# Kernel optimization log

Measured on AMD Instinct MI355X. Metric: run time of the kernel, lower is better.

## Reference

```python
import jax, jax.numpy as jnp
import numpy as np

N = 200000    # nodes
DMAX = 32     # max in-degree (padded)
F = 128       # in_feats
H = 128       # lstm hidden == in_feats (use_pp=False)
OUT = 128     # out_feats


def setup_inputs() -> dict:
    key = jax.random.key(0)
    ks = jax.random.split(key, 11)
    u = lambda k, shape, s: jax.random.uniform(k, shape, jnp.float32, -s, s)
    feat = jax.random.normal(ks[0], (N, F), jnp.float32)
    # norms come from sqrt(degree) in the original; keep them positive, O(1)
    in_norm = jax.random.uniform(ks[1], (N,), jnp.float32) + 1.0
    out_norm = jax.random.uniform(ks[2], (N,), jnp.float32) + 1.0
    neighbors = jax.random.randint(ks[3], (N, DMAX), 0, N, jnp.int32)
    degrees = jax.random.randint(ks[4], (N,), 1, DMAX + 1, jnp.int32)
    s_lstm = 1.0 / np.sqrt(H)   # torch LSTM default init scale
    s_lin = 1.0 / np.sqrt(F)    # module's reset_parameters scale
    W_ih = u(ks[5], (4 * H, F), s_lstm)
    W_hh = u(ks[6], (4 * H, H), s_lstm)
    b_ih = u(ks[7], (4 * H,), s_lstm)
    b_hh = u(ks[8], (4 * H,), s_lstm)
    W_lin = u(ks[9], (OUT, F), s_lin)
    b_lin = u(ks[10], (OUT,), s_lin)
    return dict(feat=feat, in_norm=in_norm, out_norm=out_norm,
                W_ih=W_ih, W_hh=W_hh, b_ih=b_ih, b_hh=b_hh,
                W_lin=W_lin, b_lin=b_lin,
                neighbors=neighbors, degrees=degrees)


def reference(feat, in_norm, out_norm, W_ih, W_hh, b_ih, b_hh, W_lin, b_lin,
              neighbors, degrees):
    # graph.nodes['_U'].data['h'] = feat / out_norm
    msg_src = feat / out_norm[:, None]                      # [N, F]
    n, dmax = neighbors.shape
    h_dim = W_hh.shape[1]
    step_mask = jnp.arange(dmax)[None, :] < degrees[:, None]  # [N, DMAX]

    def step(carry, xs):
        h, c = carry
        idx_t, m_t = xs                                      # [N], [N]
        x = msg_src[idx_t]                                   # gather messages [N, F]
        gates = x @ W_ih.T + b_ih + h @ W_hh.T + b_hh        # [N, 4H]
        i, f, g, o = jnp.split(gates, 4, axis=-1)
        i = jax.nn.sigmoid(i)
        f = jax.nn.sigmoid(f)
        o = jax.nn.sigmoid(o)
        g = jnp.tanh(g)
        c_new = f * c + i * g
        h_new = o * jnp.tanh(c_new)
        m = m_t[:, None]
        return (jnp.where(m, h_new, h), jnp.where(m, c_new, c)), None

    init = (jnp.zeros((n, h_dim), feat.dtype), jnp.zeros((n, h_dim), feat.dtype))
    (h_final, _), _ = jax.lax.scan(step, init, (neighbors.T, step_mask.T))
    # feat = linear(h / in_norm)
    return (h_final / in_norm[:, None]) @ W_lin.T + b_lin
```

## Files before the change

kernel.cpp:

```cpp
#include <hip/hip_runtime.h>

#define NN 200000
#define NB 64
#define NWG (NN / NB)

typedef unsigned short u16;
typedef unsigned int u32;
typedef __attribute__((ext_vector_type(8))) short short8;
typedef __attribute__((ext_vector_type(4))) float f32x4;

#define LOG2E 1.4426950408889634f
#define TWOLOG2E 2.8853900817779268f

__device__ __forceinline__ u16 f2bf(float x) {
  u32 u = __float_as_uint(x);
  u += 0x7FFFu + ((u >> 16) & 1u);
  return (u16)(u >> 16);
}

__global__ void k_prep_msg(const float* __restrict__ feat, const float* __restrict__ onorm,
                           u16* __restrict__ msg) {
  int i = blockIdx.x * 256 + threadIdx.x;
  int row = i >> 4, c8 = (i & 15) * 8;
  const float4 a = *(const float4*)(feat + (size_t)row * 128 + c8);
  const float4 b = *(const float4*)(feat + (size_t)row * 128 + c8 + 4);
  float s = 1.0f / onorm[row];
  short8 v = { (short)f2bf(a.x * s), (short)f2bf(a.y * s), (short)f2bf(a.z * s), (short)f2bf(a.w * s),
               (short)f2bf(b.x * s), (short)f2bf(b.y * s), (short)f2bf(b.z * s), (short)f2bf(b.w * s) };
  *(short8*)(msg + (size_t)row * 128 + c8) = v;
}

__global__ void k_prep_w(const float* __restrict__ Wih, const float* __restrict__ Whh,
                         const float* __restrict__ Wlin, const float* __restrict__ bih,
                         const float* __restrict__ bhh, u16* __restrict__ wihb,
                         u16* __restrict__ whhb, u16* __restrict__ wlinb,
                         float* __restrict__ bsum) {
  int i = blockIdx.x * 256 + threadIdx.x;
  if (i < 65536) {
    int gate = i >> 14;
    float s = (gate == 2) ? TWOLOG2E : -LOG2E;
    wihb[i] = f2bf(Wih[i] * s);
  } else if (i < 131072) {
    int j = i - 65536;
    int gate = j >> 14;
    float s = (gate == 2) ? TWOLOG2E : -LOG2E;
    whhb[j] = f2bf(Whh[j] * s);
  } else if (i < 147456) {
    wlinb[i - 131072] = f2bf(Wlin[i - 131072]);
  } else {
    int j = i - 147456;
    float s = ((j >> 7) == 2) ? TWOLOG2E : -LOG2E;
    bsum[j] = (bih[j] + bhh[j]) * s;
  }
}

__global__ void k_hist(const int* __restrict__ degs, int* __restrict__ hist, int n) {
  __shared__ int lh[33];
  if (threadIdx.x < 33) lh[threadIdx.x] = 0;
  __syncthreads();
  int i = blockIdx.x * 256 + threadIdx.x;
  if (i < n) atomicAdd(&lh[degs[i]], 1);
  __syncthreads();
  if (threadIdx.x < 33 && lh[threadIdx.x]) atomicAdd(&hist[threadIdx.x], lh[threadIdx.x]);
}

__global__ void k_scan(const int* __restrict__ hist, int* __restrict__ basep) {
  if (threadIdx.x == 0 && blockIdx.x == 0) {
    int a = 0;
    for (int d = 32; d >= 1; --d) { basep[d] = a; a += hist[d]; }
    basep[0] = a;
  }
}

__global__ void k_scatter(const int* __restrict__ degs, int* __restrict__ basep,
                          int* __restrict__ perm, int n) {
  __shared__ int lh[33], lbase[33], lc[33];
  int t = threadIdx.x;
  if (t < 33) { lh[t] = 0; lc[t] = 0; }
  __syncthreads();
  int i = blockIdx.x * 256 + t;
  int d = (i < n) ? degs[i] : 0;
  if (i < n) atomicAdd(&lh[d], 1);
  __syncthreads();
  if (t < 33 && lh[t]) lbase[t] = atomicAdd(&basep[t], lh[t]);
  __syncthreads();
  if (i < n) { int r = atomicAdd(&lc[d], 1); perm[lbase[d] + r] = i; }
}

__global__ __launch_bounds__(512, 2) void k_main(
    const u16* __restrict__ msg, const u16* __restrict__ wihb,
    const u16* __restrict__ whhb, const u16* __restrict__ wlinb,
    const float* __restrict__ bsum, const float* __restrict__ blin,
    const float* __restrict__ inorm, const int* __restrict__ nbrs,
    const int* __restrict__ degs, const int* __restrict__ perm,
    float* __restrict__ out) {
  __shared__ alignas(16) u16 Xl[2][64 * 136];
  __shared__ alignas(16) u16 Hl[2][64 * 136];
  __shared__ int gidl[64];

  const int tid = threadIdx.x;
  const int w = tid >> 6;
  const int lane = tid & 63;
  const int l15 = lane & 15;
  const int g4 = lane >> 4;
  const int w16 = w * 16;
  const int gr = tid >> 4;
  const int gc = (tid & 15) * 8;
  const int base = blockIdx.x * NB;

  if (tid < NB) gidl[tid] = perm[base + tid];
  {
    u32* hz = (u32*)Hl[0];
#pragma unroll
    for (int s = 0; s < 8; ++s) hz[tid + s * 512] = 0;
    if (tid < 256) hz[tid + 4096] = 0;
  }
  __syncthreads();

  const int gid0 = gidl[gr], gid1 = gidl[gr + 32];
  const int* nb0 = nbrs + (size_t)gid0 * 32;
  const int* nb1 = nbrs + (size_t)gid1 * 32;

  short8 fih[4][4], fhh[4][4];
#pragma unroll
  for (int g = 0; g < 4; ++g)
#pragma unroll
    for (int kk = 0; kk < 4; ++kk) {
      size_t o = (size_t)(g * 128 + w16 + l15) * 128 + kk * 32 + g4 * 8;
      fih[g][kk] = *(const short8*)(wihb + o);
      fhh[g][kk] = *(const short8*)(whhb + o);
    }
  float bias[4];
#pragma unroll
  for (int g = 0; g < 4; ++g) bias[g] = bsum[g * 128 + w16 + l15];

  u32 dgp[4];
#pragma unroll
  for (int r = 0; r < 4; ++r) {
    u32 p = 0;
#pragma unroll
    for (int q = 0; q < 4; ++q) p |= ((u32)degs[gidl[r * 16 + g4 * 4 + q]]) << (8 * q);
    dgp[r] = p;
  }
  const int maxdeg = degs[gidl[0]];

  {
    int i0 = nb0[0], i1 = nb1[0];
    short8 p0 = *(const short8*)(msg + (size_t)i0 * 128 + gc);
    short8 p1 = *(const short8*)(msg + (size_t)i1 * 128 + gc);
    *(short8*)(&Xl[0][gr * 136 + gc]) = p0;
    *(short8*)(&Xl[0][(gr + 32) * 136 + gc]) = p1;
  }
  int ni0 = 0, ni1 = 0;
  if (maxdeg > 1) { ni0 = nb0[1]; ni1 = nb1[1]; }

  float c[4][4] = {};
  u16 hbf[4][4] = {};
  __syncthreads();

  int cur = 0;
  for (int t = 0; t < maxdeg; ++t) {
    const int nxt = cur ^ 1;
    short8 pf0, pf1;
    if (t + 1 < maxdeg) {
      pf0 = *(const short8*)(msg + (size_t)ni0 * 128 + gc);
      pf1 = *(const short8*)(msg + (size_t)ni1 * 128 + gc);
    }
    if (t + 2 < maxdeg) { ni0 = nb0[t + 2]; ni1 = nb1[t + 2]; }

    const u16* Xc = &Xl[cur][0];
    const u16* Hc = &Hl[cur][0];

#pragma unroll
    for (int rp = 0; rp < 2; ++rp) {
      f32x4 acc[2][4];
#pragma unroll
      for (int r = 0; r < 2; ++r)
#pragma unroll
        for (int g = 0; g < 4; ++g) acc[r][g] = (f32x4){bias[g], bias[g], bias[g], bias[g]};

#pragma unroll
      for (int rf = 0; rf < 2; ++rf) {
        short8 ax[4];
#pragma unroll
        for (int kk = 0; kk < 4; ++kk)
          ax[kk] = *(const short8*)(&Xc[(rp * 32 + rf * 16 + l15) * 136 + kk * 32 + g4 * 8]);
#pragma unroll
        for (int kk = 0; kk < 4; ++kk)
#pragma unroll
          for (int g = 0; g < 4; ++g)
            acc[rf][g] = __builtin_amdgcn_mfma_f32_16x16x32_bf16(ax[kk], fih[g][kk], acc[rf][g], 0, 0, 0);
      }
#pragma unroll
      for (int rf = 0; rf < 2; ++rf) {
        short8 ah[4];
#pragma unroll
        for (int kk = 0; kk < 4; ++kk)
          ah[kk] = *(const short8*)(&Hc[(rp * 32 + rf * 16 + l15) * 136 + kk * 32 + g4 * 8]);
#pragma unroll
        for (int kk = 0; kk < 4; ++kk)
#pragma unroll
          for (int g = 0; g < 4; ++g)
            acc[rf][g] = __builtin_amdgcn_mfma_f32_16x16x32_bf16(ah[kk], fhh[g][kk], acc[rf][g], 0, 0, 0);
      }

#pragma unroll
      for (int r = 0; r < 2; ++r) {
        const int rr = rp * 2 + r;
#pragma unroll
        for (int q = 0; q < 4; ++q) {
          float ei = __builtin_amdgcn_exp2f(acc[r][0][q]);
          float ef = __builtin_amdgcn_exp2f(acc[r][1][q]);
          float eg = __builtin_amdgcn_exp2f(acc[r][2][q]);
          float eo = __builtin_amdgcn_exp2f(acc[r][3][q]);
          float fv  = __builtin_amdgcn_rcpf(1.0f + ef);
          float rig = __builtin_amdgcn_rcpf((1.0f + ei) * (1.0f + eg));
          float ig  = (eg - 1.0f) * rig;
          float cn  = fv * c[rr][q] + ig;
          float ec  = __builtin_amdgcn_exp2f(cn * TWOLOG2E);
          float rho = __builtin_amdgcn_rcpf((1.0f + eo) * (1.0f + ec));
          float hn  = (ec - 1.0f) * rho;
          bool act = (int)((dgp[rr] >> (8 * q)) & 255u) > t;
          c[rr][q] = act ? cn : c[rr][q];
          hbf[rr][q] = act ? f2bf(hn) : hbf[rr][q];
        }
      }
    }

    if (t + 1 < maxdeg) {
      *(short8*)(&Xl[nxt][gr * 136 + gc]) = pf0;
      *(short8*)(&Xl[nxt][(gr + 32) * 136 + gc]) = pf1;
    }
#pragma unroll
    for (int rr = 0; rr < 4; ++rr)
#pragma unroll
      for (int q = 0; q < 4; ++q)
        Hl[nxt][(rr * 16 + g4 * 4 + q) * 136 + w16 + l15] = hbf[rr][q];
    __syncthreads();
    cur = nxt;
  }

  const u16* Hf = &Hl[cur][0];

  short8 wl[4];
#pragma unroll
  for (int kk = 0; kk < 4; ++kk)
    wl[kk] = *(const short8*)(wlinb + (size_t)(w16 + l15) * 128 + kk * 32 + g4 * 8);
  f32x4 a2[4] = {};
#pragma unroll
  for (int kk = 0; kk < 4; ++kk)
#pragma unroll
    for (int r = 0; r < 4; ++r) {
      short8 ah = *(const short8*)(&Hf[(r * 16 + l15) * 136 + kk * 32 + g4 * 8]);
      a2[r] = __builtin_amdgcn_mfma_f32_16x16x32_bf16(ah, wl[kk], a2[r], 0, 0, 0);
    }
  float blv = blin[w16 + l15];
#pragma unroll
  for (int r = 0; r < 4; ++r)
#pragma unroll
    for (int q = 0; q < 4; ++q) {
      int nl = r * 16 + g4 * 4 + q;
      int g = gidl[nl];
      out[(size_t)g * 128 + w16 + l15] = a2[r][q] / inorm[g] + blv;
    }
}

extern "C" void kernel_launch(void* const* d_in, const int* in_sizes, int n_in,
                              void* d_out, int out_size, void* d_ws, size_t ws_size,
                              hipStream_t stream) {
  const float* feat    = (const float*)d_in[0];
  const float* in_norm = (const float*)d_in[1];
  const float* out_nrm = (const float*)d_in[2];
  const float* W_ih    = (const float*)d_in[3];
  const float* W_hh    = (const float*)d_in[4];
  const float* b_ih    = (const float*)d_in[5];
  const float* b_hh    = (const float*)d_in[6];
  const float* W_lin   = (const float*)d_in[7];
  const float* b_lin   = (const float*)d_in[8];
  const int* neighbors = (const int*)d_in[9];
  const int* degrees   = (const int*)d_in[10];
  float* out = (float*)d_out;

  char* ws = (char*)d_ws;
  u16* msg    = (u16*)(ws);
  u16* wihb   = (u16*)(ws + 51200000);
  u16* whhb   = (u16*)(ws + 51331072);
  u16* wlinb  = (u16*)(ws + 51462144);
  float* bsum = (float*)(ws + 51494912);
  int* perm   = (int*)(ws + 51496960);
  int* hist   = (int*)(ws + 52296960);
  int* basep  = hist + 64;
  if (ws_size < 52297600) return;

  hipMemsetAsync(hist, 0, 64 * 4, stream);
  k_prep_msg<<<12500, 256, 0, stream>>>(feat, out_nrm, msg);
  k_prep_w<<<578, 256, 0, stream>>>(W_ih, W_hh, W_lin, b_ih, b_hh, wihb, whhb, wlinb, bsum);
  k_hist<<<782, 256, 0, stream>>>(degrees, hist, NN);
  k_scan<<<1, 1, 0, stream>>>(hist, basep);
  k_scatter<<<782, 256, 0, stream>>>(degrees, basep, perm, NN);
  k_main<<<NWG, 512, 0, stream>>>(msg, wihb, whhb, wlinb, bsum, b_lin, in_norm,
                                  neighbors, degrees, perm, out);
}
```

Measured before the change: 1.070 ms.

## Double LSTM node tile per workgroup and interleave gathers with MFMA row blocks

Each workgroup now processes 128 nodes instead of 64, so every block amortises its register-resident W_ih/W_hh fragments over twice as many rows. The inner loop walks 8 row blocks one at a time, raises wave priority around the MFMA sections, and spreads the next-step message gathers and LDS stores across specific row blocks. New h values are written to LDS as soon as each block finishes rather than in a batch at the end. LDS use doubles to roughly 140 KB and register pressure rises, which may cut occupancy below the two blocks per CU requested. Padding the last block and sharing one maxdeg across 128 degree-sorted nodes may also add wasted steps.

New measurement: 2.497 ms. 133% more time.

```diff
diff --git a/kernel.cpp b/kernel.cpp
--- a/kernel.cpp
+++ b/kernel.cpp
@@ -1,8 +1,8 @@
 #include <hip/hip_runtime.h>
 
 #define NN 200000
-#define NB 64
-#define NWG (NN / NB)
+#define NB 128
+#define NWG ((NN + NB - 1) / NB)
 
 typedef unsigned short u16;
 typedef unsigned int u32;
@@ -94,9 +94,9 @@
     const float* __restrict__ inorm, const int* __restrict__ nbrs,
     const int* __restrict__ degs, const int* __restrict__ perm,
     float* __restrict__ out) {
-  __shared__ alignas(16) u16 Xl[2][64 * 136];
-  __shared__ alignas(16) u16 Hl[2][64 * 136];
-  __shared__ int gidl[64];
+  __shared__ alignas(16) u16 Xl[2][128 * 136];
+  __shared__ alignas(16) u16 Hl[2][128 * 136];
+  __shared__ int gidl[128];
 
   const int tid = threadIdx.x;
   const int w = tid >> 6;
@@ -108,18 +108,23 @@
   const int gc = (tid & 15) * 8;
   const int base = blockIdx.x * NB;
 
-  if (tid < NB) gidl[tid] = perm[base + tid];
+  if (tid < NB) {
+    int idx = base + tid;
+    gidl[tid] = perm[idx < NN ? idx : NN - 1];
+  }
   {
     u32* hz = (u32*)Hl[0];
 #pragma unroll
-    for (int s = 0; s < 8; ++s) hz[tid + s * 512] = 0;
-    if (tid < 256) hz[tid + 4096] = 0;
+    for (int s = 0; s < 17; ++s) hz[tid + s * 512] = 0;
   }
   __syncthreads();
 
   const int gid0 = gidl[gr], gid1 = gidl[gr + 32];
+  const int gid2 = gidl[gr + 64], gid3 = gidl[gr + 96];
   const int* nb0 = nbrs + (size_t)gid0 * 32;
   const int* nb1 = nbrs + (size_t)gid1 * 32;
+  const int* nb2 = nbrs + (size_t)gid2 * 32;
+  const int* nb3 = nbrs + (size_t)gid3 * 32;
 
   short8 fih[4][4], fhh[4][4];
 #pragma unroll
@@ -134,9 +139,9 @@
 #pragma unroll
   for (int g = 0; g < 4; ++g) bias[g] = bsum[g * 128 + w16 + l15];
 
-  u32 dgp[4];
-#pragma unroll
-  for (int r = 0; r < 4; ++r) {
+  u32 dgp[8];
+#pragma unroll
+  for (int r = 0; r < 8; ++r) {
     u32 p = 0;
 #pragma unroll
     for (int q = 0; q < 4; ++q) p |= ((u32)degs[gidl[r * 16 + g4 * 4 + q]]) << (8 * q);
@@ -145,97 +150,107 @@
   const int maxdeg = degs[gidl[0]];
 
   {
-    int i0 = nb0[0], i1 = nb1[0];
+    int i0 = nb0[0], i1 = nb1[0], i2 = nb2[0], i3 = nb3[0];
     short8 p0 = *(const short8*)(msg + (size_t)i0 * 128 + gc);
     short8 p1 = *(const short8*)(msg + (size_t)i1 * 128 + gc);
+    short8 p2 = *(const short8*)(msg + (size_t)i2 * 128 + gc);
+    short8 p3 = *(const short8*)(msg + (size_t)i3 * 128 + gc);
     *(short8*)(&Xl[0][gr * 136 + gc]) = p0;
     *(short8*)(&Xl[0][(gr + 32) * 136 + gc]) = p1;
-  }
-  int ni0 = 0, ni1 = 0;
-  if (maxdeg > 1) { ni0 = nb0[1]; ni1 = nb1[1]; }
-
-  float c[4][4] = {};
-  u16 hbf[4][4] = {};
+    *(short8*)(&Xl[0][(gr + 64) * 136 + gc]) = p2;
+    *(short8*)(&Xl[0][(gr + 96) * 136 + gc]) = p3;
+  }
+  int ni0 = 0, ni1 = 0, ni2 = 0, ni3 = 0;
+  if (maxdeg > 1) { ni0 = nb0[1]; ni1 = nb1[1]; ni2 = nb2[1]; ni3 = nb3[1]; }
+
+  float c[8][4] = {};
+  u32 hpk[8][2] = {};
   __syncthreads();
 
   int cur = 0;
   for (int t = 0; t < maxdeg; ++t) {
     const int nxt = cur ^ 1;
-    short8 pf0, pf1;
-    if (t + 1 < maxdeg) {
+    const bool more = (t + 1 < maxdeg);
+    short8 pf0, pf1, pf2, pf3;
+    if (more) {
       pf0 = *(const short8*)(msg + (size_t)ni0 * 128 + gc);
       pf1 = *(const short8*)(msg + (size_t)ni1 * 128 + gc);
     }
-    if (t + 2 < maxdeg) { ni0 = nb0[t + 2]; ni1 = nb1[t + 2]; }
-
     const u16* Xc = &Xl[cur][0];
     const u16* Hc = &Hl[cur][0];
-
-#pragma unroll
-    for (int rp = 0; rp < 2; ++rp) {
-      f32x4 acc[2][4];
-#pragma unroll
-      for (int r = 0; r < 2; ++r)
-#pragma unroll
-        for (int g = 0; g < 4; ++g) acc[r][g] = (f32x4){bias[g], bias[g], bias[g], bias[g]};
-
-#pragma unroll
-      for (int rf = 0; rf < 2; ++rf) {
+    u16* Xn = &Xl[nxt][0];
+    u16* Hn = &Hl[nxt][0];
+
+#pragma unroll
+    for (int rf = 0; rf < 8; ++rf) {
+      f32x4 acc[4];
+#pragma unroll
+      for (int g = 0; g < 4; ++g) acc[g] = (f32x4){bias[g], bias[g], bias[g], bias[g]};
+
+      __builtin_amdgcn_s_setprio(1);
+      {
         short8 ax[4];
 #pragma unroll
         for (int kk = 0; kk < 4; ++kk)
-          ax[kk] = *(const short8*)(&Xc[(rp * 32 + rf * 16 + l15) * 136 + kk * 32 + g4 * 8]);
+          ax[kk] = *(const short8*)(&Xc[(rf * 16 + l15) * 136 + kk * 32 + g4 * 8]);
 #pragma unroll
         for (int kk = 0; kk < 4; ++kk)
 #pragma unroll
           for (int g = 0; g < 4; ++g)
-            acc[rf][g] = __builtin_amdgcn_mfma_f32_16x16x32_bf16(ax[kk], fih[g][kk], acc[rf][g], 0, 0, 0);
-      }
-#pragma unroll
-      for (int rf = 0; rf < 2; ++rf) {
+            acc[g] = __builtin_amdgcn_mfma_f32_16x16x32_bf16(ax[kk], fih[g][kk], acc[g], 0, 0, 0);
+      }
+      {
         short8 ah[4];
 #pragma unroll
         for (int kk = 0; kk < 4; ++kk)
-          ah[kk] = *(const short8*)(&Hc[(rp * 32 + rf * 16 + l15) * 136 + kk * 32 + g4 * 8]);
+          ah[kk] = *(const short8*)(&Hc[(rf * 16 + l15) * 136 + kk * 32 + g4 * 8]);
 #pragma unroll
         for (int kk = 0; kk < 4; ++kk)
 #pragma unroll
           for (int g = 0; g < 4; ++g)
-            acc[rf][g] = __builtin_amdgcn_mfma_f32_16x16x32_bf16(ah[kk], fhh[g][kk], acc[rf][g], 0, 0, 0);
-      }
-
-#pragma unroll
-      for (int r = 0; r < 2; ++r) {
-        const int rr = rp * 2 + r;
-#pragma unroll
-        for (int q = 0; q < 4; ++q) {
-          float ei = __builtin_amdgcn_exp2f(acc[r][0][q]);
-          float ef = __builtin_amdgcn_exp2f(acc[r][1][q]);
-          float eg = __builtin_amdgcn_exp2f(acc[r][2][q]);
-          float eo = __builtin_amdgcn_exp2f(acc[r][3][q]);
-          float fv  = __builtin_amdgcn_rcpf(1.0f + ef);
-          float rig = __builtin_amdgcn_rcpf((1.0f + ei) * (1.0f + eg));
-          float ig  = (eg - 1.0f) * rig;
-          float cn  = fv * c[rr][q] + ig;
-          float ec  = __builtin_amdgcn_exp2f(cn * TWOLOG2E);
-          float rho = __builtin_amdgcn_rcpf((1.0f + eo) * (1.0f + ec));
-          float hn  = (ec - 1.0f) * rho;
-          bool act = (int)((dgp[rr] >> (8 * q)) & 255u) > t;
-          c[rr][q] = act ? cn : c[rr][q];
-          hbf[rr][q] = act ? f2bf(hn) : hbf[rr][q];
+            acc[g] = __builtin_amdgcn_mfma_f32_16x16x32_bf16(ah[kk], fhh[g][kk], acc[g], 0, 0, 0);
+      }
+      __builtin_amdgcn_s_setprio(0);
+
+      if (rf == 1 && more) {
+        *(short8*)(&Xn[gr * 136 + gc]) = pf0;
+        *(short8*)(&Xn[(gr + 32) * 136 + gc]) = pf1;
+        pf2 = *(const short8*)(msg + (size_t)ni2 * 128 + gc);
+        pf3 = *(const short8*)(msg + (size_t)ni3 * 128 + gc);
+      }
+      if (rf == 4) {
+        if (more) {
+          *(short8*)(&Xn[(gr + 64) * 136 + gc]) = pf2;
+          *(short8*)(&Xn[(gr + 96) * 136 + gc]) = pf3;
         }
+        if (t + 2 < maxdeg) {
+          ni0 = nb0[t + 2]; ni1 = nb1[t + 2]; ni2 = nb2[t + 2]; ni3 = nb3[t + 2];
+        }
+      }
+
+#pragma unroll
+      for (int q = 0; q < 4; ++q) {
+        float ei = __builtin_amdgcn_exp2f(acc[0][q]);
+        float ef = __builtin_amdgcn_exp2f(acc[1][q]);
+        float eg = __builtin_amdgcn_exp2f(acc[2][q]);
+        float eo = __builtin_amdgcn_exp2f(acc[3][q]);
+        float fv  = __builtin_amdgcn_rcpf(1.0f + ef);
+        float rig = __builtin_amdgcn_rcpf((1.0f + ei) * (1.0f + eg));
+        float ig  = (eg - 1.0f) * rig;
+        float cn  = fv * c[rf][q] + ig;
+        float ec  = __builtin_amdgcn_exp2f(cn * TWOLOG2E);
+        float rho = __builtin_amdgcn_rcpf((1.0f + eo) * (1.0f + ec));
+        float hn  = (ec - 1.0f) * rho;
+        bool act = (int)((dgp[rf] >> (8 * q)) & 255u) > t;
+        c[rf][q] = act ? cn : c[rf][q];
+        u32 word = hpk[rf][q >> 1];
+        u16 oldv = (u16)(word >> ((q & 1) * 16));
+        u16 nh = act ? f2bf(hn) : oldv;
+        hpk[rf][q >> 1] = (q & 1) ? ((word & 0x0000FFFFu) | ((u32)nh << 16))
+                                  : ((word & 0xFFFF0000u) | (u32)nh);
+        Hn[(rf * 16 + g4 * 4 + q) * 136 + w16 + l15] = nh;
       }
     }
-
-    if (t + 1 < maxdeg) {
-      *(short8*)(&Xl[nxt][gr * 136 + gc]) = pf0;
-      *(short8*)(&Xl[nxt][(gr + 32) * 136 + gc]) = pf1;
-    }
-#pragma unroll
-    for (int rr = 0; rr < 4; ++rr)
-#pragma unroll
-      for (int q = 0; q < 4; ++q)
-        Hl[nxt][(rr * 16 + g4 * 4 + q) * 136 + w16 + l15] = hbf[rr][q];
     __syncthreads();
     cur = nxt;
   }
@@ -246,23 +261,26 @@
 #pragma unroll
   for (int kk = 0; kk < 4; ++kk)
     wl[kk] = *(const short8*)(wlinb + (size_t)(w16 + l15) * 128 + kk * 32 + g4 * 8);
-  f32x4 a2[4] = {};
-#pragma unroll
-  for (int kk = 0; kk < 4; ++kk)
-#pragma unroll
-    for (int r = 0; r < 4; ++r) {
-      short8 ah = *(const short8*)(&Hf[(r * 16 + l15) * 136 + kk * 32 + g4 * 8]);
-      a2[r] = __builtin_amdgcn_mfma_f32_16x16x32_bf16(ah, wl[kk], a2[r], 0, 0, 0);
-    }
   float blv = blin[w16 + l15];
 #pragma unroll
-  for (int r = 0; r < 4; ++r)
-#pragma unroll
-    for (int q = 0; q < 4; ++q) {
-      int nl = r * 16 + g4 * 4 + q;
-      int g = gidl[nl];
-      out[(size_t)g * 128 + w16 + l15] = a2[r][q] / inorm[g] + blv;
-    }
+  for (int half = 0; half < 2; ++half) {
+    f32x4 a2[4] = {};
+#pragma unroll
+    for (int kk = 0; kk < 4; ++kk)
+#pragma unroll
+      for (int r = 0; r < 4; ++r) {
+        short8 ah = *(const short8*)(&Hf[((half * 4 + r) * 16 + l15) * 136 + kk * 32 + g4 * 8]);
+        a2[r] = __builtin_amdgcn_mfma_f32_16x16x32_bf16(ah, wl[kk], a2[r], 0, 0, 0);
+      }
+#pragma unroll
+    for (int r = 0; r < 4; ++r)
+#pragma unroll
+      for (int q = 0; q < 4; ++q) {
+        int nl = (half * 4 + r) * 16 + g4 * 4 + q;
+        int g = gidl[nl];
+        out[(size_t)g * 128 + w16 + l15] = a2[r][q] / inorm[g] + blv;
+      }
+  }
 }
 
 extern "C" void kernel_launch(void* const* d_in, const int* in_sizes, int n_in,
```

## Gather messages directly into LDS with swizzled layout and early H stores

Applied to the files above, without the earlier changes.

Replaces the register-staged prefetch of neighbor message rows with direct global-to-LDS loads (global_load_lds), using an XOR-swizzled unpadded X tile so MFMA operand reads avoid bank conflicts. The initial gather is issued before the weight fragment loads to overlap latency. The hidden state is now packed into u32 registers and written to the next H buffer right after each gate computation instead of in a separate loop. This removes prefetch registers and the end-of-step LDS copy, but it relies on the per-wave 64-lane contiguous layout of the LDS DMA and adds packing arithmetic.

Result: no change. 1.059 ms (-1.0%).

```diff
diff --git a/kernel.cpp b/kernel.cpp
--- a/kernel.cpp
+++ b/kernel.cpp
@@ -16,6 +16,12 @@
   u32 u = __float_as_uint(x);
   u += 0x7FFFu + ((u >> 16) & 1u);
   return (u16)(u >> 16);
+}
+
+typedef __attribute__((address_space(3))) unsigned int lds_u32_t;
+typedef const __attribute__((address_space(1))) unsigned int glb_u32_t;
+__device__ __forceinline__ void gload16(const void* g, void* l) {
+  __builtin_amdgcn_global_load_lds((glb_u32_t*)g, (lds_u32_t*)l, 16, 0, 0);
 }
 
 __global__ void k_prep_msg(const float* __restrict__ feat, const float* __restrict__ onorm,
@@ -94,7 +100,7 @@
     const float* __restrict__ inorm, const int* __restrict__ nbrs,
     const int* __restrict__ degs, const int* __restrict__ perm,
     float* __restrict__ out) {
-  __shared__ alignas(16) u16 Xl[2][64 * 136];
+  __shared__ alignas(16) u16 Xl[2][64 * 128];
   __shared__ alignas(16) u16 Hl[2][64 * 136];
   __shared__ int gidl[64];
 
@@ -105,7 +111,8 @@
   const int g4 = lane >> 4;
   const int w16 = w * 16;
   const int gr = tid >> 4;
-  const int gc = (tid & 15) * 8;
+  const int xc8 = (((tid & 15) ^ (gr & 15)) * 8);
+  const int wbase = w * 512;
   const int base = blockIdx.x * NB;
 
   if (tid < NB) gidl[tid] = perm[base + tid];
@@ -120,6 +127,14 @@
   const int gid0 = gidl[gr], gid1 = gidl[gr + 32];
   const int* nb0 = nbrs + (size_t)gid0 * 32;
   const int* nb1 = nbrs + (size_t)gid1 * 32;
+
+  {
+    int i0 = nb0[0], i1 = nb1[0];
+    gload16(msg + (size_t)i0 * 128 + xc8, &Xl[0][wbase]);
+    gload16(msg + (size_t)i1 * 128 + xc8, &Xl[0][4096 + wbase]);
+  }
+  int ni0 = 0, ni1 = 0;
+  if (degs[gidl[0]] > 1) { ni0 = nb0[1]; ni1 = nb1[1]; }
 
   short8 fih[4][4], fhh[4][4];
 #pragma unroll
@@ -144,32 +159,26 @@
   }
   const int maxdeg = degs[gidl[0]];
 
-  {
-    int i0 = nb0[0], i1 = nb1[0];
-    short8 p0 = *(const short8*)(msg + (size_t)i0 * 128 + gc);
-    short8 p1 = *(const short8*)(msg + (size_t)i1 * 128 + gc);
-    *(short8*)(&Xl[0][gr * 136 + gc]) = p0;
-    *(short8*)(&Xl[0][(gr + 32) * 136 + gc]) = p1;
-  }
-  int ni0 = 0, ni1 = 0;
-  if (maxdeg > 1) { ni0 = nb0[1]; ni1 = nb1[1]; }
+  int xsw[4];
+#pragma unroll
+  for (int kk = 0; kk < 4; ++kk) xsw[kk] = ((kk * 4 + g4) ^ l15) * 8;
 
   float c[4][4] = {};
-  u16 hbf[4][4] = {};
+  u32 hpk[4][2] = {};
   __syncthreads();
 
   int cur = 0;
   for (int t = 0; t < maxdeg; ++t) {
     const int nxt = cur ^ 1;
-    short8 pf0, pf1;
     if (t + 1 < maxdeg) {
-      pf0 = *(const short8*)(msg + (size_t)ni0 * 128 + gc);
-      pf1 = *(const short8*)(msg + (size_t)ni1 * 128 + gc);
+      gload16(msg + (size_t)ni0 * 128 + xc8, &Xl[nxt][wbase]);
+      gload16(msg + (size_t)ni1 * 128 + xc8, &Xl[nxt][4096 + wbase]);
     }
     if (t + 2 < maxdeg) { ni0 = nb0[t + 2]; ni1 = nb1[t + 2]; }
 
     const u16* Xc = &Xl[cur][0];
     const u16* Hc = &Hl[cur][0];
+    u16* Hn = &Hl[nxt][0];
 
 #pragma unroll
     for (int rp = 0; rp < 2; ++rp) {
@@ -184,7 +193,7 @@
         short8 ax[4];
 #pragma unroll
         for (int kk = 0; kk < 4; ++kk)
-          ax[kk] = *(const short8*)(&Xc[(rp * 32 + rf * 16 + l15) * 136 + kk * 32 + g4 * 8]);
+          ax[kk] = *(const short8*)(&Xc[(rp * 32 + rf * 16 + l15) * 128 + xsw[kk]]);
 #pragma unroll
         for (int kk = 0; kk < 4; ++kk)
 #pragma unroll
@@ -222,20 +231,15 @@
           float hn  = (ec - 1.0f) * rho;
           bool act = (int)((dgp[rr] >> (8 * q)) & 255u) > t;
           c[rr][q] = act ? cn : c[rr][q];
-          hbf[rr][q] = act ? f2bf(hn) : hbf[rr][q];
+          u32 word = hpk[rr][q >> 1];
+          u16 oldv = (u16)(word >> ((q & 1) * 16));
+          u16 nh = act ? f2bf(hn) : oldv;
+          hpk[rr][q >> 1] = (q & 1) ? ((word & 0x0000FFFFu) | ((u32)nh << 16))
+                                    : ((word & 0xFFFF0000u) | (u32)nh);
+          Hn[(rr * 16 + g4 * 4 + q) * 136 + w16 + l15] = nh;
         }
       }
     }
-
-    if (t + 1 < maxdeg) {
-      *(short8*)(&Xl[nxt][gr * 136 + gc]) = pf0;
-      *(short8*)(&Xl[nxt][(gr + 32) * 136 + gc]) = pf1;
-    }
-#pragma unroll
-    for (int rr = 0; rr < 4; ++rr)
-#pragma unroll
-      for (int q = 0; q < 4; ++q)
-        Hl[nxt][(rr * 16 + g4 * 4 + q) * 136 + w16 + l15] = hbf[rr][q];
     __syncthreads();
     cur = nxt;
   }
```
